# Performance work log

Hardware: AMD Instinct MI355X
Metric: run time of the kernel (lower is better)

## Reference

```python
import jax, jax.numpy as jnp
import numpy as np

N, C, D, H, W = 4, 9, 16, 1024, 1024  # batch, grid channels, grid size, image HxW


def setup_inputs() -> dict:
    key = jax.random.key(0)
    k1, k2, k3, k4 = jax.random.split(key, 4)
    bilateral_grid = jax.random.normal(k1, (N, C, D, D, D), dtype=jnp.float32)
    guidemap = jax.random.uniform(k2, (N, 3, H, W), dtype=jnp.float32)
    conv_w = jax.random.normal(k3, (3, C + 3), dtype=jnp.float32) * 0.1  # 1x1 conv kernel
    conv_b = jax.random.normal(k4, (3,), dtype=jnp.float32) * 0.1
    return {"bilateral_grid": bilateral_grid, "guidemap": guidemap,
            "conv_w": conv_w, "conv_b": conv_b}


def _trilinear_slice(grid, guide):
    # grid: [N, C, D, D, D]; guide: [N, 3, H, W] with values in [0,1]
    n, c, d = grid.shape[0], grid.shape[1], grid.shape[2]
    h, w = guide.shape[2], guide.shape[3]
    grid_flat = grid.reshape(n, c, d * d * d)
    coords = jnp.clip(guide, 0.0, 1.0) * (d - 1)          # [N,3,H,W]
    i0 = jnp.clip(jnp.floor(coords), 0, d - 2).astype(jnp.int32)
    f = coords - i0.astype(coords.dtype)                   # fractional part
    r0, g0, b0 = i0[:, 0], i0[:, 1], i0[:, 2]              # [N,H,W]
    fr, fg, fb = f[:, 0], f[:, 1], f[:, 2]                 # [N,H,W]

    def gather(ir, ig, ib):
        flat = ((ir * d + ig) * d + ib).reshape(n, 1, h * w)
        return jnp.take_along_axis(grid_flat, flat, axis=2)  # [N,C,H*W]

    out = jnp.zeros((n, c, h * w), dtype=grid.dtype)
    for dr in (0, 1):
        for dg in (0, 1):
            for db in (0, 1):
                wgt = ((fr if dr else 1.0 - fr) *
                       (fg if dg else 1.0 - fg) *
                       (fb if db else 1.0 - fb)).reshape(n, 1, h * w)
                out = out + gather(r0 + dr, g0 + dg, b0 + db) * wgt
    return out.reshape(n, c, h, w)


def reference(bilateral_grid, guidemap, conv_w, conv_b):
    res = _trilinear_slice(bilateral_grid, guidemap)       # [N,9,H,W]
    res = jnp.concatenate([res, guidemap], axis=1)         # [N,12,H,W]
    out = jnp.einsum('oi,nihw->nohw', conv_w, res) + conv_b[None, :, None, None]
    return out
```

## Files before the change

kernel.cpp:

```cpp
#include <hip/hip_runtime.h>

static constexpr int N_ = 4;
static constexpr int C_ = 9;
static constexpr int D_ = 16;
static constexpr int HWp = 1024 * 1024;
static constexpr int CELLS = D_ * D_ * D_;
static constexpr int PT = HWp / 4;
static constexpr int TPB = 512;
static constexpr int BPI = 256;

__global__ __launch_bounds__(256) void fold_grid_kernel(
    const float* __restrict__ grid, const float* __restrict__ cw,
    float4* __restrict__ pre)
{
    int t = blockIdx.x * blockDim.x + threadIdx.x;
    if (t >= N_ * CELLS) return;
    int n = t >> 12;
    int cell = t & (CELLS - 1);
    const float* g = grid + ((size_t)n * C_) * CELLS + cell;
    float a0 = 0.f, a1 = 0.f, a2 = 0.f;
#pragma unroll
    for (int c = 0; c < C_; ++c) {
        float v = g[(size_t)c * CELLS];
        a0 = fmaf(cw[c], v, a0);
        a1 = fmaf(cw[12 + c], v, a1);
        a2 = fmaf(cw[24 + c], v, a2);
    }
    pre[t] = make_float4(a0, a1, a2, 0.f);
}

__device__ __forceinline__ float4 f4lerp(const float4 a, const float4 b, float t) {
    return make_float4(fmaf(b.x - a.x, t, a.x),
                       fmaf(b.y - a.y, t, a.y),
                       fmaf(b.z - a.z, t, a.z),
                       0.f);
}

__global__ __launch_bounds__(TPB) void slice_kernel(
    const float* __restrict__ guide, const float4* __restrict__ pre,
    const float* __restrict__ cw, const float* __restrict__ cbias,
    float* __restrict__ out)
{
    __shared__ float4 sPre[CELLS];

    const int n  = blockIdx.x >> 8;
    const int bi = blockIdx.x & (BPI - 1);

    const float4* __restrict__ P = pre + (size_t)n * CELLS;
#pragma unroll
    for (int i = 0; i < CELLS / TPB; ++i)
        sPre[i * TPB + threadIdx.x] = P[i * TPB + threadIdx.x];
    __syncthreads();

    const float4* gR = (const float4*)(guide + (size_t)(n * 3 + 0) * HWp);
    const float4* gG = (const float4*)(guide + (size_t)(n * 3 + 1) * HWp);
    const float4* gB = (const float4*)(guide + (size_t)(n * 3 + 2) * HWp);
    float4* oR = (float4*)(out + (size_t)(n * 3 + 0) * HWp);
    float4* oG = (float4*)(out + (size_t)(n * 3 + 1) * HWp);
    float4* oB = (float4*)(out + (size_t)(n * 3 + 2) * HWp);

    const float w0r = cw[9],  w0g = cw[10], w0b = cw[11];
    const float w1r = cw[21], w1g = cw[22], w1b = cw[23];
    const float w2r = cw[33], w2g = cw[34], w2b = cw[35];
    const float bi0 = cbias[0], bi1 = cbias[1], bi2 = cbias[2];

    for (int p4 = bi * TPB + threadIdx.x; p4 < PT; p4 += BPI * TPB) {
        float4 r4 = gR[p4];
        float4 g4 = gG[p4];
        float4 b4 = gB[p4];

        float rr[4] = {r4.x, r4.y, r4.z, r4.w};
        float gg[4] = {g4.x, g4.y, g4.z, g4.w};
        float bb[4] = {b4.x, b4.y, b4.z, b4.w};
        float o0[4], o1[4], o2[4];

#pragma unroll
        for (int j = 0; j < 4; ++j) {
            float cr = fminf(fmaxf(rr[j], 0.f), 1.f) * 15.f;
            float cg = fminf(fmaxf(gg[j], 0.f), 1.f) * 15.f;
            float cb = fminf(fmaxf(bb[j], 0.f), 1.f) * 15.f;
            int ir = min((int)cr, 14);
            int ig = min((int)cg, 14);
            int ib = min((int)cb, 14);
            float fr = cr - (float)ir;
            float fg = cg - (float)ig;
            float fb = cb - (float)ib;
            int base = (ir * 16 + ig) * 16 + ib;

            float4 c000 = sPre[base];
            float4 c001 = sPre[base + 1];
            float4 c010 = sPre[base + 16];
            float4 c011 = sPre[base + 17];
            float4 c100 = sPre[base + 256];
            float4 c101 = sPre[base + 257];
            float4 c110 = sPre[base + 272];
            float4 c111 = sPre[base + 273];

            float4 v00 = f4lerp(c000, c001, fb);
            float4 v01 = f4lerp(c010, c011, fb);
            float4 v10 = f4lerp(c100, c101, fb);
            float4 v11 = f4lerp(c110, c111, fb);
            float4 v0  = f4lerp(v00, v01, fg);
            float4 v1  = f4lerp(v10, v11, fg);
            float4 v   = f4lerp(v0, v1, fr);

            o0[j] = v.x + fmaf(w0r, rr[j], fmaf(w0g, gg[j], fmaf(w0b, bb[j], bi0)));
            o1[j] = v.y + fmaf(w1r, rr[j], fmaf(w1g, gg[j], fmaf(w1b, bb[j], bi1)));
            o2[j] = v.z + fmaf(w2r, rr[j], fmaf(w2g, gg[j], fmaf(w2b, bb[j], bi2)));
        }

        oR[p4] = make_float4(o0[0], o0[1], o0[2], o0[3]);
        oG[p4] = make_float4(o1[0], o1[1], o1[2], o1[3]);
        oB[p4] = make_float4(o2[0], o2[1], o2[2], o2[3]);
    }
}

extern "C" void kernel_launch(void* const* d_in, const int* in_sizes, int n_in,
                              void* d_out, int out_size, void* d_ws, size_t ws_size,
                              hipStream_t stream) {
    const float* grid  = (const float*)d_in[0];
    const float* guide = (const float*)d_in[1];
    const float* cw    = (const float*)d_in[2];
    const float* cb    = (const float*)d_in[3];
    float* out  = (float*)d_out;
    float4* pre = (float4*)d_ws;

    fold_grid_kernel<<<(N_ * CELLS + 255) / 256, 256, 0, stream>>>(grid, cw, pre);

    slice_kernel<<<N_ * BPI, TPB, 0, stream>>>(guide, pre, cw, cb, out);
}
```

Before: 123.2 us.

## Pack folded grid as bf16 in LDS and use nontemporal guide/output access

The pre-folded 3-channel grid is stored as bf16 packed into 8 bytes per cell instead of a 16-byte float4. This halves the shared-memory footprint per block, which together with a launch-bounds occupancy hint is meant to allow more resident blocks, and it halves the LDS traffic for the eight corner reads. Guide loads and output stores switch to nontemporal builtins to avoid cache pollution on the streaming data. Rounding the folded grid to bf16 adds precision loss that may exceed tolerance.

Result: slower. 160.9 us (+30.6%).

```diff
diff --git a/kernel.cpp b/kernel.cpp
--- a/kernel.cpp
+++ b/kernel.cpp
@@ -1,4 +1,5 @@
 #include <hip/hip_runtime.h>
+#include <hip/hip_bf16.h>
 
 static constexpr int N_ = 4;
 static constexpr int C_ = 9;
@@ -9,9 +10,11 @@
 static constexpr int TPB = 512;
 static constexpr int BPI = 256;
 
+typedef float fx4 __attribute__((ext_vector_type(4)));
+
 __global__ __launch_bounds__(256) void fold_grid_kernel(
     const float* __restrict__ grid, const float* __restrict__ cw,
-    float4* __restrict__ pre)
+    uint2* __restrict__ pre)
 {
     int t = blockIdx.x * blockDim.x + threadIdx.x;
     if (t >= N_ * CELLS) return;
@@ -26,38 +29,50 @@
         a1 = fmaf(cw[12 + c], v, a1);
         a2 = fmaf(cw[24 + c], v, a2);
     }
-    pre[t] = make_float4(a0, a1, a2, 0.f);
+    unsigned short b0 = __bfloat16_as_ushort(__float2bfloat16(a0));
+    unsigned short b1 = __bfloat16_as_ushort(__float2bfloat16(a1));
+    unsigned short b2 = __bfloat16_as_ushort(__float2bfloat16(a2));
+    uint2 v;
+    v.x = (unsigned)b0 | ((unsigned)b1 << 16);
+    v.y = (unsigned)b2;
+    pre[t] = v;
 }
 
-__device__ __forceinline__ float4 f4lerp(const float4 a, const float4 b, float t) {
-    return make_float4(fmaf(b.x - a.x, t, a.x),
-                       fmaf(b.y - a.y, t, a.y),
-                       fmaf(b.z - a.z, t, a.z),
-                       0.f);
+__device__ __forceinline__ void unpack3(uint2 w, float& x, float& y, float& z) {
+    x = __uint_as_float(w.x << 16);
+    y = __uint_as_float(w.x & 0xFFFF0000u);
+    z = __uint_as_float(w.y << 16);
 }
 
-__global__ __launch_bounds__(TPB) void slice_kernel(
-    const float* __restrict__ guide, const float4* __restrict__ pre,
+__device__ __forceinline__ float lerp1(float a, float b, float t) {
+    return fmaf(b - a, t, a);
+}
+
+__global__ __launch_bounds__(TPB, 6) void slice_kernel(
+    const float* __restrict__ guide, const uint2* __restrict__ pre,
     const float* __restrict__ cw, const float* __restrict__ cbias,
     float* __restrict__ out)
 {
-    __shared__ float4 sPre[CELLS];
+    __shared__ uint2 sPre[CELLS];
 
     const int n  = blockIdx.x >> 8;
     const int bi = blockIdx.x & (BPI - 1);
 
-    const float4* __restrict__ P = pre + (size_t)n * CELLS;
+    {
+        const uint4* src = (const uint4*)(pre + (size_t)n * CELLS);
+        uint4* dst = (uint4*)sPre;
 #pragma unroll
-    for (int i = 0; i < CELLS / TPB; ++i)
-        sPre[i * TPB + threadIdx.x] = P[i * TPB + threadIdx.x];
+        for (int i = 0; i < (CELLS / 2) / TPB; ++i)
+            dst[i * TPB + threadIdx.x] = src[i * TPB + threadIdx.x];
+    }
     __syncthreads();
 
-    const float4* gR = (const float4*)(guide + (size_t)(n * 3 + 0) * HWp);
-    const float4* gG = (const float4*)(guide + (size_t)(n * 3 + 1) * HWp);
-    const float4* gB = (const float4*)(guide + (size_t)(n * 3 + 2) * HWp);
-    float4* oR = (float4*)(out + (size_t)(n * 3 + 0) * HWp);
-    float4* oG = (float4*)(out + (size_t)(n * 3 + 1) * HWp);
-    float4* oB = (float4*)(out + (size_t)(n * 3 + 2) * HWp);
+    const fx4* gR = (const fx4*)(guide + (size_t)(n * 3 + 0) * HWp);
+    const fx4* gG = (const fx4*)(guide + (size_t)(n * 3 + 1) * HWp);
+    const fx4* gB = (const fx4*)(guide + (size_t)(n * 3 + 2) * HWp);
+    fx4* oR = (fx4*)(out + (size_t)(n * 3 + 0) * HWp);
+    fx4* oG = (fx4*)(out + (size_t)(n * 3 + 1) * HWp);
+    fx4* oB = (fx4*)(out + (size_t)(n * 3 + 2) * HWp);
 
     const float w0r = cw[9],  w0g = cw[10], w0b = cw[11];
     const float w1r = cw[21], w1g = cw[22], w1b = cw[23];
@@ -65,9 +80,9 @@
     const float bi0 = cbias[0], bi1 = cbias[1], bi2 = cbias[2];
 
     for (int p4 = bi * TPB + threadIdx.x; p4 < PT; p4 += BPI * TPB) {
-        float4 r4 = gR[p4];
-        float4 g4 = gG[p4];
-        float4 b4 = gB[p4];
+        fx4 r4 = __builtin_nontemporal_load(&gR[p4]);
+        fx4 g4 = __builtin_nontemporal_load(&gG[p4]);
+        fx4 b4 = __builtin_nontemporal_load(&gB[p4]);
 
         float rr[4] = {r4.x, r4.y, r4.z, r4.w};
         float gg[4] = {g4.x, g4.y, g4.z, g4.w};
@@ -87,31 +102,50 @@
             float fb = cb - (float)ib;
             int base = (ir * 16 + ig) * 16 + ib;
 
-            float4 c000 = sPre[base];
-            float4 c001 = sPre[base + 1];
-            float4 c010 = sPre[base + 16];
-            float4 c011 = sPre[base + 17];
-            float4 c100 = sPre[base + 256];
-            float4 c101 = sPre[base + 257];
-            float4 c110 = sPre[base + 272];
-            float4 c111 = sPre[base + 273];
+            uint2 q000 = sPre[base];
+            uint2 q001 = sPre[base + 1];
+            uint2 q010 = sPre[base + 16];
+            uint2 q011 = sPre[base + 17];
+            uint2 q100 = sPre[base + 256];
+            uint2 q101 = sPre[base + 257];
+            uint2 q110 = sPre[base + 272];
+            uint2 q111 = sPre[base + 273];
 
-            float4 v00 = f4lerp(c000, c001, fb);
-            float4 v01 = f4lerp(c010, c011, fb);
-            float4 v10 = f4lerp(c100, c101, fb);
-            float4 v11 = f4lerp(c110, c111, fb);
-            float4 v0  = f4lerp(v00, v01, fg);
-            float4 v1  = f4lerp(v10, v11, fg);
-            float4 v   = f4lerp(v0, v1, fr);
+            float ax, ay, az, bx, by, bz;
+            float v00x, v00y, v00z, v01x, v01y, v01z;
+            float v10x, v10y, v10z, v11x, v11y, v11z;
 
-            o0[j] = v.x + fmaf(w0r, rr[j], fmaf(w0g, gg[j], fmaf(w0b, bb[j], bi0)));
-            o1[j] = v.y + fmaf(w1r, rr[j], fmaf(w1g, gg[j], fmaf(w1b, bb[j], bi1)));
-            o2[j] = v.z + fmaf(w2r, rr[j], fmaf(w2g, gg[j], fmaf(w2b, bb[j], bi2)));
+            unpack3(q000, ax, ay, az); unpack3(q001, bx, by, bz);
+            v00x = lerp1(ax, bx, fb); v00y = lerp1(ay, by, fb); v00z = lerp1(az, bz, fb);
+            unpack3(q010, ax, ay, az); unpack3(q011, bx, by, bz);
+            v01x = lerp1(ax, bx, fb); v01y = lerp1(ay, by, fb); v01z = lerp1(az, bz, fb);
+            unpack3(q100, ax, ay, az); unpack3(q101, bx, by, bz);
+            v10x = lerp1(ax, bx, fb); v10y = lerp1(ay, by, fb); v10z = lerp1(az, bz, fb);
+            unpack3(q110, ax, ay, az); unpack3(q111, bx, by, bz);
+            v11x = lerp1(ax, bx, fb); v11y = lerp1(ay, by, fb); v11z = lerp1(az, bz, fb);
+
+            float v0x = lerp1(v00x, v01x, fg);
+            float v0y = lerp1(v00y, v01y, fg);
+            float v0z = lerp1(v00z, v01z, fg);
+            float v1x = lerp1(v10x, v11x, fg);
+            float v1y = lerp1(v10y, v11y, fg);
+            float v1z = lerp1(v10z, v11z, fg);
+
+            float vx = lerp1(v0x, v1x, fr);
+            float vy = lerp1(v0y, v1y, fr);
+            float vz = lerp1(v0z, v1z, fr);
+
+            o0[j] = vx + fmaf(w0r, rr[j], fmaf(w0g, gg[j], fmaf(w0b, bb[j], bi0)));
+            o1[j] = vy + fmaf(w1r, rr[j], fmaf(w1g, gg[j], fmaf(w1b, bb[j], bi1)));
+            o2[j] = vz + fmaf(w2r, rr[j], fmaf(w2g, gg[j], fmaf(w2b, bb[j], bi2)));
         }
 
-        oR[p4] = make_float4(o0[0], o0[1], o0[2], o0[3]);
-        oG[p4] = make_float4(o1[0], o1[1], o1[2], o1[3]);
-        oB[p4] = make_float4(o2[0], o2[1], o2[2], o2[3]);
+        fx4 s0 = {o0[0], o0[1], o0[2], o0[3]};
+        fx4 s1 = {o1[0], o1[1], o1[2], o1[3]};
+        fx4 s2 = {o2[0], o2[1], o2[2], o2[3]};
+        __builtin_nontemporal_store(s0, &oR[p4]);
+        __builtin_nontemporal_store(s1, &oG[p4]);
+        __builtin_nontemporal_store(s2, &oB[p4]);
     }
 }
 
@@ -122,8 +156,8 @@
     const float* guide = (const float*)d_in[1];
     const float* cw    = (const float*)d_in[2];
     const float* cb    = (const float*)d_in[3];
-    float* out  = (float*)d_out;
-    float4* pre = (float4*)d_ws;
+    float* out = (float*)d_out;
+    uint2* pre = (uint2*)d_ws;
 
     fold_grid_kernel<<<(N_ * CELLS + 255) / 256, 256, 0, stream>>>(grid, cw, pre);
 
```
